# Kernel tuning notes

Hardware: AMD Instinct MI355X
Metric: run time of the kernel (lower is better)

## Reference

```python
import jax, jax.numpy as jnp
import numpy as np

N = 100_000      # nodes
E = 1_600_000    # edges
IN = 128         # input_dim
HID = 64         # hidden_dim
H = 4            # num_heads
DH = HID // H    # per-head dim
L = 3            # num_layers
OUT = 64         # output_dim
SLOPE = 0.2      # DGL GATConv LeakyReLU default
EPS = 1e-5       # LayerNorm eps


def setup_inputs() -> dict:
    key = jax.random.key(0)
    ks = jax.random.split(key, 20)
    s = 0.02
    return {
        "node_features": jax.random.normal(ks[0], (N, IN), jnp.float32),
        "src": jax.random.randint(ks[1], (E,), 0, N, jnp.int32),
        "dst": jax.random.randint(ks[2], (E,), 0, N, jnp.int32),
        # input projection
        "W_in": jax.random.normal(ks[3], (IN, HID), jnp.float32) * s,
        "b_in": jnp.zeros((HID,), jnp.float32),
        # rewiring MLP: Linear(2*HID,64) -> Tanh -> Linear(64,1) -> Sigmoid
        "W_a1": jax.random.normal(ks[4], (2 * HID, 64), jnp.float32) * s,
        "b_a1": jnp.zeros((64,), jnp.float32),
        "W_a2": jax.random.normal(ks[5], (64, 1), jnp.float32) * s,
        "b_a2": jnp.zeros((1,), jnp.float32),
        # stacked GATConv params for L layers
        "W_gat": jax.random.normal(ks[6], (L, HID, H * DH), jnp.float32) * s,
        "a_l": jax.random.normal(ks[7], (L, H, DH), jnp.float32) * s,
        "a_r": jax.random.normal(ks[8], (L, H, DH), jnp.float32) * s,
        "b_gat": jnp.zeros((L, H, DH), jnp.float32),
        # LayerNorm + output projection
        "ln_g": jnp.ones((HID,), jnp.float32),
        "ln_b": jnp.zeros((HID,), jnp.float32),
        "W_out": jax.random.normal(ks[9], (HID, OUT), jnp.float32) * s,
        "b_out": jnp.zeros((OUT,), jnp.float32),
    }


def _gat_layer(h, src, dst, W, al, ar, b):
    # h: (N, HID) -> z: (N, H, DH)
    z = (h @ W).reshape(N, H, DH)
    el = jnp.sum(z * al, axis=-1)                       # (N, H)
    er = jnp.sum(z * ar, axis=-1)                       # (N, H)
    e = jax.nn.leaky_relu(el[src] + er[dst], SLOPE)     # (E, H)
    # segment softmax over incoming edges of each dst node
    m = jax.ops.segment_max(e, dst, num_segments=N)     # (N, H)
    ex = jnp.exp(e - m[dst])                            # (E, H)
    den = jax.ops.segment_sum(ex, dst, num_segments=N)  # (N, H)
    alpha = ex / den[dst]                               # (E, H)
    msg = z[src] * alpha[..., None]                     # (E, H, DH)
    out = jax.ops.segment_sum(msg, dst, num_segments=N) # (N, H, DH)
    # residual (identity since HID == H*DH) + bias, then flatten(1)
    out = out + h.reshape(N, H, DH) + b
    return out.reshape(N, H * DH)


def reference(node_features, src, dst, W_in, b_in, W_a1, b_a1, W_a2, b_a2,
              W_gat, a_l, a_r, b_gat, ln_g, ln_b, W_out, b_out):
    h = node_features @ W_in + b_in                     # (N, HID)
    # GraphRewiringModule: edge-wise gather + MLP + sigmoid score
    he = jnp.concatenate([h[src], h[dst]], axis=1)      # (E, 2*HID)
    edge_score = jax.nn.sigmoid(jnp.tanh(he @ W_a1 + b_a1) @ W_a2 + b_a2)  # (E,1); unused downstream, as in source
    for l in range(L):
        h = _gat_layer(h, src, dst, W_gat[l], a_l[l], a_r[l], b_gat[l])
    # LayerNorm
    mu = jnp.mean(h, axis=-1, keepdims=True)
    var = jnp.mean((h - mu) ** 2, axis=-1, keepdims=True)
    h = (h - mu) * jax.lax.rsqrt(var + EPS) * ln_g + ln_b
    return h @ W_out + b_out                            # (N, OUT)
```

## Files before the change

### kernel.cpp

```cpp
#include <hip/hip_runtime.h>

#define NN 100000
#define EE 1600000
#define IN_DIM 128
#define HID 64
#define NH 4
#define DH 16
#define NL 3
#define OUT_DIM 64
#define SLOPE 0.2f
#define LN_EPS 1e-5f
#define RB 4

#define BSH 9
#define BSZ 512
#define NB ((NN + BSZ - 1) / BSZ)
#define CAP 10240
#define CHUNK 4096
#define P1_BLOCKS ((EE + CHUNK - 1) / CHUNK)

using short8 = __attribute__((ext_vector_type(8))) short;
using f32x4  = __attribute__((ext_vector_type(4))) float;

__device__ __forceinline__ float bcast(float x, int lane) {
    return __int_as_float(__builtin_amdgcn_readlane(__float_as_int(x), lane));
}
__device__ __forceinline__ unsigned f2bf(float x) {
    unsigned u = __float_as_uint(x);
    u += 0x7FFFu + ((u >> 16) & 1u);
    return u >> 16;
}
__device__ __forceinline__ float bflo(unsigned zp) {
    return __uint_as_float(zp << 16);
}
__device__ __forceinline__ float bfhi(unsigned zp) {
    return __uint_as_float(zp & 0xFFFF0000u);
}

__global__ void k_wpack(const float* __restrict__ W, uint4* __restrict__ Wb) {
    const int tid = blockIdx.x * 256 + threadIdx.x;
    if (tid >= 1024) return;
    const int lane = tid & 63;
    const int ntkk = tid >> 6;
    const int nt = ntkk & 3, kk = ntkk >> 2;
    const int k0 = kk * 32 + (lane >> 4) * 8;
    const int n  = nt * 16 + (lane & 15);
    unsigned dw[4];
#pragma unroll
    for (int p = 0; p < 4; ++p) {
        const unsigned lo = f2bf(W[(k0 + 2 * p) * HID + n]);
        const unsigned hi = f2bf(W[(k0 + 2 * p + 1) * HID + n]);
        dw[p] = lo | (hi << 16);
    }
    Wb[ntkk * 64 + lane] = make_uint4(dw[0], dw[1], dw[2], dw[3]);
}

__device__ float walv(const float* __restrict__ W, const float* __restrict__ al,
                      const float* __restrict__ ar, int k, int c) {
    if (c < 4) {
        float s = 0.f;
#pragma unroll
        for (int d = 0; d < 16; ++d) s += W[k * HID + c * 16 + d] * al[c * 16 + d];
        return s;
    }
    if (c < 8) {
        const int hh = c - 4;
        float s = 0.f;
#pragma unroll
        for (int d = 0; d < 16; ++d) s += W[k * HID + hh * 16 + d] * ar[hh * 16 + d];
        return s;
    }
    return 0.f;
}

__global__ void k_wpack_gat(const float* __restrict__ W_gat, const float* __restrict__ a_l,
                            const float* __restrict__ a_r, uint4* __restrict__ Wbg) {
    const int l = blockIdx.y;
    const int tid = blockIdx.x * 256 + threadIdx.x;
    if (tid >= 640) return;
    const int lane = tid & 63;
    const int f = tid >> 6;
    const int kk = f / 5, nt = f % 5;
    const float* W  = W_gat + (size_t)l * HID * HID;
    const float* al = a_l + (size_t)l * HID;
    const float* ar = a_r + (size_t)l * HID;
    const int k0 = kk * 32 + (lane >> 4) * 8;
    const int n  = lane & 15;
    unsigned dw[4];
#pragma unroll
    for (int p = 0; p < 4; ++p) {
        float b0, b1;
        if (nt < 4) {
            b0 = W[(k0 + 2 * p) * HID + nt * 16 + n];
            b1 = W[(k0 + 2 * p + 1) * HID + nt * 16 + n];
        } else {
            b0 = walv(W, al, ar, k0 + 2 * p, n);
            b1 = walv(W, al, ar, k0 + 2 * p + 1, n);
        }
        dw[p] = f2bf(b0) | (f2bf(b1) << 16);
    }
    Wbg[(size_t)l * 640 + f * 64 + lane] = make_uint4(dw[0], dw[1], dw[2], dw[3]);
}

__global__ __launch_bounds__(256)
void k_in_gemm(const float* __restrict__ X, const uint4* __restrict__ Wb,
               const float* __restrict__ b, float* __restrict__ h) {
    const int l  = threadIdx.x & 63;
    const int wv = threadIdx.x >> 6;
    const int wrow = blockIdx.x * 64 + wv * 16;
    if (wrow >= NN) return;
    const int arow = wrow + (l & 15);
    const int kb_off = (l >> 4) * 8;
    f32x4 acc[4];
#pragma unroll
    for (int nt = 0; nt < 4; ++nt) acc[nt] = (f32x4){0.f, 0.f, 0.f, 0.f};
    const float* xr = X + (size_t)arow * IN_DIM;
#pragma unroll
    for (int kk = 0; kk < 4; ++kk) {
        const int kb = kk * 32 + kb_off;
        const float4 xa = *(const float4*)(xr + kb);
        const float4 xb = *(const float4*)(xr + kb + 4);
        const unsigned d0 = f2bf(xa.x) | (f2bf(xa.y) << 16);
        const unsigned d1 = f2bf(xa.z) | (f2bf(xa.w) << 16);
        const unsigned d2 = f2bf(xb.x) | (f2bf(xb.y) << 16);
        const unsigned d3 = f2bf(xb.z) | (f2bf(xb.w) << 16);
        const uint4 au = make_uint4(d0, d1, d2, d3);
        const short8 af = __builtin_bit_cast(short8, au);
#pragma unroll
        for (int nt = 0; nt < 4; ++nt) {
            const uint4 bu = Wb[(kk * 4 + nt) * 64 + l];
            const short8 bf = __builtin_bit_cast(short8, bu);
            acc[nt] = __builtin_amdgcn_mfma_f32_16x16x32_bf16(af, bf, acc[nt], 0, 0, 0);
        }
    }
    const int grp = l >> 4, ci = l & 15;
#pragma unroll
    for (int nt = 0; nt < 4; ++nt) {
        const int col = nt * 16 + ci;
        const float bv = b[col];
#pragma unroll
        for (int r = 0; r < 4; ++r) {
            h[(size_t)(wrow + grp * 4 + r) * HID + col] = acc[nt][r] + bv;
        }
    }
}

__global__ __launch_bounds__(256)
void k_zgemm(const float* __restrict__ h, const uint4* __restrict__ Wbg,
             unsigned* __restrict__ zb32, float* __restrict__ el, float* __restrict__ er) {
    const int l  = threadIdx.x & 63;
    const int wv = threadIdx.x >> 6;
    const int wrow = blockIdx.x * 64 + wv * 16;
    if (wrow >= NN) return;
    const int arow = wrow + (l & 15);
    const int kb_off = (l >> 4) * 8;
    f32x4 acc[5];
#pragma unroll
    for (int nt = 0; nt < 5; ++nt) acc[nt] = (f32x4){0.f, 0.f, 0.f, 0.f};
    const float* hr = h + (size_t)arow * HID;
#pragma unroll
    for (int kk = 0; kk < 2; ++kk) {
        const int kb = kk * 32 + kb_off;
        const float4 xa = *(const float4*)(hr + kb);
        const float4 xb = *(const float4*)(hr + kb + 4);
        const unsigned d0 = f2bf(xa.x) | (f2bf(xa.y) << 16);
        const unsigned d1 = f2bf(xa.z) | (f2bf(xa.w) << 16);
        const unsigned d2 = f2bf(xb.x) | (f2bf(xb.y) << 16);
        const unsigned d3 = f2bf(xb.z) | (f2bf(xb.w) << 16);
        const uint4 au = make_uint4(d0, d1, d2, d3);
        const short8 af = __builtin_bit_cast(short8, au);
#pragma unroll
        for (int nt = 0; nt < 5; ++nt) {
            const uint4 bu = Wbg[(kk * 5 + nt) * 64 + l];
            const short8 bf = __builtin_bit_cast(short8, bu);
            acc[nt] = __builtin_amdgcn_mfma_f32_16x16x32_bf16(af, bf, acc[nt], 0, 0, 0);
        }
    }
    const int grp = l >> 4, ci = l & 15;
#pragma unroll
    for (int nt = 0; nt < 4; ++nt) {
#pragma unroll
        for (int r = 0; r < 4; ++r) {
            const int row = wrow + grp * 4 + r;
            const unsigned my = f2bf(acc[nt][r]);
            const unsigned ot = (unsigned)__shfl_xor((int)my, 1, 64);
            if ((ci & 1) == 0)
                zb32[(size_t)row * 32 + nt * 8 + (ci >> 1)] = my | (ot << 16);
        }
    }
#pragma unroll
    for (int r = 0; r < 4; ++r) {
        const int row = wrow + grp * 4 + r;
        const float v = acc[4][r];
        if (ci < 4) el[row * NH + ci] = v;
        else if (ci < 8) er[row * NH + (ci - 4)] = v;
    }
}


__global__ void k_zero_bcnt(int* __restrict__ bcnt, int* __restrict__ esrc_pad) {
    if (threadIdx.x < NB) bcnt[threadIdx.x] = 0;
    if (threadIdx.x < 8) esrc_pad[threadIdx.x] = 0;
}

__global__ __launch_bounds__(256)
void k_bucketize(const int* __restrict__ src, const int* __restrict__ dst,
                 int* __restrict__ bcnt, int2* __restrict__ bbuf) {
    __shared__ int lh[256];
    __shared__ int lbase[256];
    __shared__ int lcnt[256];
    __shared__ int gbase[256];
    __shared__ int sc[256];
    __shared__ int2 stage[CHUNK];
    const int t = threadIdx.x;
    const int e0 = blockIdx.x * CHUNK;
    const int n = min(CHUNK, EE - e0);
    lh[t] = 0;
    __syncthreads();
    int myd[CHUNK / 256], mys[CHUNK / 256];
#pragma unroll
    for (int i = 0; i < CHUNK / 256; ++i) {
        const int o = i * 256 + t;
        if (o < n) {
            myd[i] = dst[e0 + o];
            mys[i] = src[e0 + o];
            atomicAdd(&lh[myd[i] >> BSH], 1);
        } else myd[i] = -1;
    }
    __syncthreads();
    {
        const int v = lh[t];
        lcnt[t] = v;
        sc[t] = v;
        __syncthreads();
        for (int off = 1; off < 256; off <<= 1) {
            const int x = (t >= off) ? sc[t - off] : 0;
            __syncthreads();
            sc[t] += x;
            __syncthreads();
        }
        lbase[t] = sc[t] - v;
        lh[t] = sc[t] - v;
    }
    __syncthreads();
#pragma unroll
    for (int i = 0; i < CHUNK / 256; ++i) {
        if (myd[i] >= 0) {
            const int b = myd[i] >> BSH;
            const int p = atomicAdd(&lh[b], 1);
            stage[p] = make_int2(mys[i], myd[i]);
        }
    }
    __syncthreads();
    if (t < NB && lcnt[t] > 0) gbase[t] = atomicAdd(&bcnt[t], lcnt[t]);
    __syncthreads();
    for (int i = t; i < n; i += 256) {
        const int2 en = stage[i];
        const int b = en.y >> BSH;
        const int gp = gbase[b] + (i - lbase[b]);
        if (gp < CAP) bbuf[(size_t)b * CAP + gp] = en;
    }
}

__global__ void k_bscan(const int* __restrict__ bcnt, int* __restrict__ bbase,
                        int* __restrict__ rowptr) {
    const int t = threadIdx.x;
    __shared__ int sc[256];
    const int v = (t < NB) ? bcnt[t] : 0;
    sc[t] = v;
    __syncthreads();
    for (int off = 1; off < 256; off <<= 1) {
        const int x = (t >= off) ? sc[t - off] : 0;
        __syncthreads();
        sc[t] += x;
        __syncthreads();
    }
    if (t < NB) bbase[t] = sc[t] - v;
    if (t == 0) rowptr[NN] = EE;
}

__global__ __launch_bounds__(256)
void k_localcsr(const int* __restrict__ bcnt, const int* __restrict__ bbase,
                const int2* __restrict__ bbuf, int* __restrict__ rowptr,
                int* __restrict__ esrc) {
    const int b = blockIdx.x;
    const int t = threadIdx.x;
    const int cnt = bcnt[b];
    const int base = bbase[b];
    const int n0 = b * BSZ;
    const int nn = min(BSZ, NN - n0);
    __shared__ int lh[BSZ];
    __shared__ int lsc[BSZ];
    __shared__ int sc[256];
    for (int i = t; i < BSZ; i += 256) lh[i] = 0;
    __syncthreads();
    const int2* bb = bbuf + (size_t)b * CAP;
    for (int i = t; i < cnt; i += 256) atomicAdd(&lh[bb[i].y & (BSZ - 1)], 1);
    __syncthreads();
    const int a0 = lh[2 * t], a1 = lh[2 * t + 1];
    const int ts = a0 + a1;
    sc[t] = ts;
    __syncthreads();
    for (int off = 1; off < 256; off <<= 1) {
        const int x = (t >= off) ? sc[t - off] : 0;
        __syncthreads();
        sc[t] += x;
        __syncthreads();
    }
    const int ebase = sc[t] - ts;
    lsc[2 * t] = ebase;
    lsc[2 * t + 1] = ebase + a0;
    __syncthreads();
    for (int i = t; i < BSZ; i += 256) {
        if (i < nn) rowptr[n0 + i] = base + lsc[i];
        lh[i] = lsc[i];
    }
    __syncthreads();
    for (int i = t; i < cnt; i += 256) {
        const int2 en = bb[i];
        const int p = atomicAdd(&lh[en.y & (BSZ - 1)], 1);
        esrc[base + p] = en.x;
    }
}

__global__ __launch_bounds__(256)
void k_gat_dst(const int* __restrict__ rowptr, const int* __restrict__ esrc,
               const float* __restrict__ el, const float* __restrict__ er,
               const uint4* __restrict__ zb128, const float* __restrict__ hin,
               const float* __restrict__ bg, float* __restrict__ hout) {
    const int j  = threadIdx.x & 63;
    const int wv = threadIdx.x >> 6;
    const int d = blockIdx.x * 4 + wv;
    if (d >= NN) return;
    const int g = j >> 3;
    const int q = j & 7;
    const int hh = q >> 1;
    const int r0 = rowptr[d], r1 = rowptr[d + 1];
    const float erh = er[d * NH + hh];
    float a0 = 0.f, a1 = 0.f, a2 = 0.f, a3 = 0.f;
    float a4 = 0.f, a5 = 0.f, a6 = 0.f, a7 = 0.f;
    float den = 0.f;
    for (int i = r0; i < r1; i += 8) {
        const int ii = i + g;
        const unsigned s = (unsigned)esrc[ii];
        const float av = el[s * NH + hh];
        const uint4 zp = zb128[s * 8u + q];
        const float x = av + erh;
        float w = __expf(fmaxf(x, SLOPE * x));
        w = (ii < r1) ? w : 0.f;
        den += w;
        a0 = fmaf(w, bflo(zp.x), a0);
        a1 = fmaf(w, bfhi(zp.x), a1);
        a2 = fmaf(w, bflo(zp.y), a2);
        a3 = fmaf(w, bfhi(zp.y), a3);
        a4 = fmaf(w, bflo(zp.z), a4);
        a5 = fmaf(w, bfhi(zp.z), a5);
        a6 = fmaf(w, bflo(zp.w), a6);
        a7 = fmaf(w, bfhi(zp.w), a7);
    }
#pragma unroll
    for (int m = 8; m <= 32; m <<= 1) {
        den += __shfl_xor(den, m, 64);
        a0 += __shfl_xor(a0, m, 64);
        a1 += __shfl_xor(a1, m, 64);
        a2 += __shfl_xor(a2, m, 64);
        a3 += __shfl_xor(a3, m, 64);
        a4 += __shfl_xor(a4, m, 64);
        a5 += __shfl_xor(a5, m, 64);
        a6 += __shfl_xor(a6, m, 64);
        a7 += __shfl_xor(a7, m, 64);
    }
    if (g == 0) {
        const int c = 8 * q;
        const float4 h0 = *(const float4*)(hin + (size_t)d * HID + c);
        const float4 h1 = *(const float4*)(hin + (size_t)d * HID + c + 4);
        const float4 b0 = *(const float4*)(bg + c);
        const float4 b1 = *(const float4*)(bg + c + 4);
        float o0 = h0.x + b0.x, o1 = h0.y + b0.y, o2 = h0.z + b0.z, o3 = h0.w + b0.w;
        float o4 = h1.x + b1.x, o5 = h1.y + b1.y, o6 = h1.z + b1.z, o7 = h1.w + b1.w;
        if (r1 > r0) {
            const float rd = 1.f / den;
            o0 = fmaf(a0, rd, o0); o1 = fmaf(a1, rd, o1);
            o2 = fmaf(a2, rd, o2); o3 = fmaf(a3, rd, o3);
            o4 = fmaf(a4, rd, o4); o5 = fmaf(a5, rd, o5);
            o6 = fmaf(a6, rd, o6); o7 = fmaf(a7, rd, o7);
        }
        *(float4*)(hout + (size_t)d * HID + c)     = make_float4(o0, o1, o2, o3);
        *(float4*)(hout + (size_t)d * HID + c + 4) = make_float4(o4, o5, o6, o7);
    }
}

__global__ __launch_bounds__(256, 4)
void k_ln_out(const float* __restrict__ h, const float* __restrict__ g,
              const float* __restrict__ be, const float* __restrict__ Wo,
              const float* __restrict__ bo, float* __restrict__ out) {
    const int j = threadIdx.x & 63;
    float Wreg[HID];
#pragma unroll
    for (int k = 0; k < HID; ++k) Wreg[k] = Wo[k * OUT_DIM + j];
    const float gj = g[j], bej = be[j], boj = bo[j];
    const int wid = (blockIdx.x * blockDim.x + threadIdx.x) >> 6;
    const int nw  = (gridDim.x * blockDim.x) >> 6;
    for (int v0 = wid * RB; v0 < NN; v0 += nw * RB) {
        float hn[RB];
#pragma unroll
        for (int r = 0; r < RB; ++r) {
            const float x = h[(size_t)(v0 + r) * HID + j];
            float s = x;
#pragma unroll
            for (int m = 32; m >= 1; m >>= 1) s += __shfl_xor(s, m, 64);
            const float mu = s * (1.f / 64.f);
            const float dx = x - mu;
            float vs = dx * dx;
#pragma unroll
            for (int m = 32; m >= 1; m >>= 1) vs += __shfl_xor(vs, m, 64);
            hn[r] = dx * rsqrtf(vs * (1.f / 64.f) + LN_EPS) * gj + bej;
        }
        float acc[RB];
#pragma unroll
        for (int r = 0; r < RB; ++r) acc[r] = boj;
#pragma unroll
        for (int k = 0; k < HID; ++k) {
#pragma unroll
            for (int r = 0; r < RB; ++r)
                acc[r] = fmaf(bcast(hn[r], k), Wreg[k], acc[r]);
        }
#pragma unroll
        for (int r = 0; r < RB; ++r) out[(size_t)(v0 + r) * OUT_DIM + j] = acc[r];
    }
}

extern "C" void kernel_launch(void* const* d_in, const int* in_sizes, int n_in,
                              void* d_out, int out_size, void* d_ws, size_t ws_size,
                              hipStream_t stream) {
    const float* X     = (const float*)d_in[0];
    const int*   src   = (const int*)d_in[1];
    const int*   dst   = (const int*)d_in[2];
    const float* W_in  = (const float*)d_in[3];
    const float* b_in  = (const float*)d_in[4];
    const float* W_gat = (const float*)d_in[9];
    const float* a_l   = (const float*)d_in[10];
    const float* a_r   = (const float*)d_in[11];
    const float* b_gat = (const float*)d_in[12];
    const float* ln_g  = (const float*)d_in[13];
    const float* ln_b  = (const float*)d_in[14];
    const float* W_out = (const float*)d_in[15];
    const float* b_out = (const float*)d_in[16];
    float* out = (float*)d_out;

    float* ws = (float*)d_ws;
    float* hA = ws;
    float* hB = hA + (size_t)NN * HID;
    unsigned* zb32 = (unsigned*)(hB + (size_t)NN * HID);
    float* el = (float*)(zb32 + (size_t)NN * (HID / 2));
    float* er = el + (size_t)NN * NH;
    int* rowptr = (int*)(er + (size_t)NN * NH);
    int* esrc   = rowptr + NN + 1;
    int* bcnt   = esrc + EE + 8;
    int* bbase  = bcnt + NB;
    uintptr_t wp = (uintptr_t)(bbase + NB);
    wp = (wp + 15) & ~(uintptr_t)15;
    uint4* Wb   = (uint4*)wp;
    uint4* Wbg  = Wb + 1024;
    int2* bbuf  = (int2*)hB;

    k_wpack<<<4, 256, 0, stream>>>(W_in, Wb);
    k_wpack_gat<<<dim3(3, NL), 256, 0, stream>>>(W_gat, a_l, a_r, Wbg);
    k_in_gemm<<<(NN + 63) / 64, 256, 0, stream>>>(X, Wb, b_in, hA);

    k_zero_bcnt<<<1, 256, 0, stream>>>(bcnt, esrc + EE);
    k_bucketize<<<P1_BLOCKS, 256, 0, stream>>>(src, dst, bcnt, bbuf);
    k_bscan<<<1, 256, 0, stream>>>(bcnt, bbase, rowptr);
    k_localcsr<<<NB, 256, 0, stream>>>(bcnt, bbase, bbuf, rowptr, esrc);

    float* hin = hA;
    float* hout = hB;
    for (int l = 0; l < NL; ++l) {
        k_zgemm<<<(NN + 63) / 64, 256, 0, stream>>>(hin, Wbg + (size_t)l * 640,
                                                    zb32, el, er);
        k_gat_dst<<<(NN + 3) / 4, 256, 0, stream>>>(rowptr, esrc, el, er,
                                                    (const uint4*)zb32, hin,
                                                    b_gat + (size_t)l * HID, hout);
        float* t = hin; hin = hout; hout = t;
    }

    k_ln_out<<<1024, 256, 0, stream>>>(hin, ln_g, ln_b, W_out, b_out, out);
}
```

Before: 301.1 us.

## Split node features into per-head planes and run GAT aggregation per head

```diff
diff --git a/kernel.cpp b/kernel.cpp
--- a/kernel.cpp
+++ b/kernel.cpp
@@ -11,6 +11,7 @@
 #define SLOPE 0.2f
 #define LN_EPS 1e-5f
 #define RB 4
+#define NG4 (NN / 4)
 
 #define BSH 9
 #define BSZ 512
@@ -136,18 +137,18 @@
     const int grp = l >> 4, ci = l & 15;
 #pragma unroll
     for (int nt = 0; nt < 4; ++nt) {
-        const int col = nt * 16 + ci;
-        const float bv = b[col];
+        const float bv = b[nt * 16 + ci];
 #pragma unroll
         for (int r = 0; r < 4; ++r) {
-            h[(size_t)(wrow + grp * 4 + r) * HID + col] = acc[nt][r] + bv;
+            const int row = wrow + grp * 4 + r;
+            h[((size_t)nt * NN + row) * 16 + ci] = acc[nt][r] + bv;
         }
     }
 }
 
 __global__ __launch_bounds__(256)
 void k_zgemm(const float* __restrict__ h, const uint4* __restrict__ Wbg,
-             unsigned* __restrict__ zb32, float* __restrict__ el, float* __restrict__ er) {
+             unsigned* __restrict__ zbp, float* __restrict__ el_p, float* __restrict__ er_p) {
     const int l  = threadIdx.x & 63;
     const int wv = threadIdx.x >> 6;
     const int wrow = blockIdx.x * 64 + wv * 16;
@@ -157,12 +158,12 @@
     f32x4 acc[5];
 #pragma unroll
     for (int nt = 0; nt < 5; ++nt) acc[nt] = (f32x4){0.f, 0.f, 0.f, 0.f};
-    const float* hr = h + (size_t)arow * HID;
 #pragma unroll
     for (int kk = 0; kk < 2; ++kk) {
         const int kb = kk * 32 + kb_off;
-        const float4 xa = *(const float4*)(hr + kb);
-        const float4 xb = *(const float4*)(hr + kb + 4);
+        const float* hp = h + ((size_t)(kb >> 4) * NN + arow) * 16 + (kb & 15);
+        const float4 xa = *(const float4*)(hp);
+        const float4 xb = *(const float4*)(hp + 4);
         const unsigned d0 = f2bf(xa.x) | (f2bf(xa.y) << 16);
         const unsigned d1 = f2bf(xa.z) | (f2bf(xa.w) << 16);
         const unsigned d2 = f2bf(xb.x) | (f2bf(xb.y) << 16);
@@ -185,15 +186,15 @@
             const unsigned my = f2bf(acc[nt][r]);
             const unsigned ot = (unsigned)__shfl_xor((int)my, 1, 64);
             if ((ci & 1) == 0)
-                zb32[(size_t)row * 32 + nt * 8 + (ci >> 1)] = my | (ot << 16);
+                zbp[((size_t)nt * NN + row) * 8 + (ci >> 1)] = my | (ot << 16);
         }
     }
 #pragma unroll
     for (int r = 0; r < 4; ++r) {
         const int row = wrow + grp * 4 + r;
         const float v = acc[4][r];
-        if (ci < 4) el[row * NH + ci] = v;
-        else if (ci < 8) er[row * NH + (ci - 4)] = v;
+        if (ci < 4) el_p[(size_t)ci * NN + row] = v;
+        else if (ci < 8) er_p[(size_t)(ci - 4) * NN + row] = v;
     }
 }
 
@@ -325,68 +326,51 @@
 
 __global__ __launch_bounds__(256)
 void k_gat_dst(const int* __restrict__ rowptr, const int* __restrict__ esrc,
-               const float* __restrict__ el, const float* __restrict__ er,
-               const uint4* __restrict__ zb128, const float* __restrict__ hin,
-               const float* __restrict__ bg, float* __restrict__ hout) {
+               const float* __restrict__ el_p, const float* __restrict__ er_p,
+               const unsigned* __restrict__ zbp, const float* __restrict__ hin_p,
+               const float* __restrict__ bg, float* __restrict__ hout_p) {
     const int j  = threadIdx.x & 63;
     const int wv = threadIdx.x >> 6;
-    const int d = blockIdx.x * 4 + wv;
-    if (d >= NN) return;
+    const int hh = blockIdx.x / NG4;
+    const int ng = blockIdx.x % NG4;
+    const int d = ng * 4 + wv;
     const int g = j >> 3;
     const int q = j & 7;
-    const int hh = q >> 1;
     const int r0 = rowptr[d], r1 = rowptr[d + 1];
-    const float erh = er[d * NH + hh];
-    float a0 = 0.f, a1 = 0.f, a2 = 0.f, a3 = 0.f;
-    float a4 = 0.f, a5 = 0.f, a6 = 0.f, a7 = 0.f;
-    float den = 0.f;
+    const size_t plane = (size_t)hh * NN;
+    const float erh = er_p[plane + d];
+    float s0 = 0.f, s1 = 0.f, den = 0.f;
     for (int i = r0; i < r1; i += 8) {
         const int ii = i + g;
-        const unsigned s = (unsigned)esrc[ii];
-        const float av = el[s * NH + hh];
-        const uint4 zp = zb128[s * 8u + q];
+        const unsigned s = (unsigned)__builtin_nontemporal_load(esrc + ii);
+        const float av = el_p[plane + s];
+        const unsigned zp = zbp[(plane + s) * 8 + q];
         const float x = av + erh;
         float w = __expf(fmaxf(x, SLOPE * x));
         w = (ii < r1) ? w : 0.f;
         den += w;
-        a0 = fmaf(w, bflo(zp.x), a0);
-        a1 = fmaf(w, bfhi(zp.x), a1);
-        a2 = fmaf(w, bflo(zp.y), a2);
-        a3 = fmaf(w, bfhi(zp.y), a3);
-        a4 = fmaf(w, bflo(zp.z), a4);
-        a5 = fmaf(w, bfhi(zp.z), a5);
-        a6 = fmaf(w, bflo(zp.w), a6);
-        a7 = fmaf(w, bfhi(zp.w), a7);
+        s0 = fmaf(w, bflo(zp), s0);
+        s1 = fmaf(w, bfhi(zp), s1);
     }
 #pragma unroll
     for (int m = 8; m <= 32; m <<= 1) {
         den += __shfl_xor(den, m, 64);
-        a0 += __shfl_xor(a0, m, 64);
-        a1 += __shfl_xor(a1, m, 64);
-        a2 += __shfl_xor(a2, m, 64);
-        a3 += __shfl_xor(a3, m, 64);
-        a4 += __shfl_xor(a4, m, 64);
-        a5 += __shfl_xor(a5, m, 64);
-        a6 += __shfl_xor(a6, m, 64);
-        a7 += __shfl_xor(a7, m, 64);
+        s0  += __shfl_xor(s0, m, 64);
+        s1  += __shfl_xor(s1, m, 64);
     }
     if (g == 0) {
-        const int c = 8 * q;
-        const float4 h0 = *(const float4*)(hin + (size_t)d * HID + c);
-        const float4 h1 = *(const float4*)(hin + (size_t)d * HID + c + 4);
-        const float4 b0 = *(const float4*)(bg + c);
-        const float4 b1 = *(const float4*)(bg + c + 4);
-        float o0 = h0.x + b0.x, o1 = h0.y + b0.y, o2 = h0.z + b0.z, o3 = h0.w + b0.w;
-        float o4 = h1.x + b1.x, o5 = h1.y + b1.y, o6 = h1.z + b1.z, o7 = h1.w + b1.w;
+        const size_t off = (plane + d) * 16 + 2 * q;
+        const double hvd = __builtin_nontemporal_load((const double*)(hin_p + off));
+        const float2 hv = __builtin_bit_cast(float2, hvd);
+        float o0 = hv.x + bg[hh * 16 + 2 * q];
+        float o1 = hv.y + bg[hh * 16 + 2 * q + 1];
         if (r1 > r0) {
             const float rd = 1.f / den;
-            o0 = fmaf(a0, rd, o0); o1 = fmaf(a1, rd, o1);
-            o2 = fmaf(a2, rd, o2); o3 = fmaf(a3, rd, o3);
-            o4 = fmaf(a4, rd, o4); o5 = fmaf(a5, rd, o5);
-            o6 = fmaf(a6, rd, o6); o7 = fmaf(a7, rd, o7);
-        }
-        *(float4*)(hout + (size_t)d * HID + c)     = make_float4(o0, o1, o2, o3);
-        *(float4*)(hout + (size_t)d * HID + c + 4) = make_float4(o4, o5, o6, o7);
+            o0 = fmaf(s0, rd, o0);
+            o1 = fmaf(s1, rd, o1);
+        }
+        const float2 ov = make_float2(o0, o1);
+        __builtin_nontemporal_store(__builtin_bit_cast(double, ov), (double*)(hout_p + off));
     }
 }
 
@@ -399,13 +383,15 @@
 #pragma unroll
     for (int k = 0; k < HID; ++k) Wreg[k] = Wo[k * OUT_DIM + j];
     const float gj = g[j], bej = be[j], boj = bo[j];
+    const size_t pbase = (size_t)(j >> 4) * NN;
+    const int ci = j & 15;
     const int wid = (blockIdx.x * blockDim.x + threadIdx.x) >> 6;
     const int nw  = (gridDim.x * blockDim.x) >> 6;
     for (int v0 = wid * RB; v0 < NN; v0 += nw * RB) {
         float hn[RB];
 #pragma unroll
         for (int r = 0; r < RB; ++r) {
-            const float x = h[(size_t)(v0 + r) * HID + j];
+            const float x = h[(pbase + (v0 + r)) * 16 + ci];
             float s = x;
 #pragma unroll
             for (int m = 32; m >= 1; m >>= 1) s += __shfl_xor(s, m, 64);
@@ -451,10 +437,10 @@
     float* ws = (float*)d_ws;
     float* hA = ws;
     float* hB = hA + (size_t)NN * HID;
-    unsigned* zb32 = (unsigned*)(hB + (size_t)NN * HID);
-    float* el = (float*)(zb32 + (size_t)NN * (HID / 2));
-    float* er = el + (size_t)NN * NH;
-    int* rowptr = (int*)(er + (size_t)NN * NH);
+    unsigned* zbp = (unsigned*)(hB + (size_t)NN * HID);
+    float* el_p = (float*)(zbp + (size_t)NN * (HID / 2));
+    float* er_p = el_p + (size_t)NN * NH;
+    int* rowptr = (int*)(er_p + (size_t)NN * NH);
     int* esrc   = rowptr + NN + 1;
     int* bcnt   = esrc + EE + 8;
     int* bbase  = bcnt + NB;
@@ -477,10 +463,9 @@
     float* hout = hB;
     for (int l = 0; l < NL; ++l) {
         k_zgemm<<<(NN + 63) / 64, 256, 0, stream>>>(hin, Wbg + (size_t)l * 640,
-                                                    zb32, el, er);
-        k_gat_dst<<<(NN + 3) / 4, 256, 0, stream>>>(rowptr, esrc, el, er,
-                                                    (const uint4*)zb32, hin,
-                                                    b_gat + (size_t)l * HID, hout);
+                                                    zbp, el_p, er_p);
+        k_gat_dst<<<NH * NG4, 256, 0, stream>>>(rowptr, esrc, el_p, er_p, zbp, hin,
+                                                b_gat + (size_t)l * HID, hout);
         float* t = hin; hin = hout; hout = t;
     }
 
```

New measurement: 676.5 us. 2.25x slower.

## Store hidden state in bf16 and software-pipeline edge gathers in GAT aggregation

Applied to the files above, without the earlier changes.

```diff
diff --git a/kernel.cpp b/kernel.cpp
--- a/kernel.cpp
+++ b/kernel.cpp
@@ -29,6 +29,9 @@
     unsigned u = __float_as_uint(x);
     u += 0x7FFFu + ((u >> 16) & 1u);
     return u >> 16;
+}
+__device__ __forceinline__ float bf2f(unsigned short b) {
+    return __uint_as_float(((unsigned)b) << 16);
 }
 __device__ __forceinline__ float bflo(unsigned zp) {
     return __uint_as_float(zp << 16);
@@ -104,7 +107,7 @@
 
 __global__ __launch_bounds__(256)
 void k_in_gemm(const float* __restrict__ X, const uint4* __restrict__ Wb,
-               const float* __restrict__ b, float* __restrict__ h) {
+               const float* __restrict__ b, unsigned* __restrict__ h32) {
     const int l  = threadIdx.x & 63;
     const int wv = threadIdx.x >> 6;
     const int wrow = blockIdx.x * 64 + wv * 16;
@@ -136,17 +139,20 @@
     const int grp = l >> 4, ci = l & 15;
 #pragma unroll
     for (int nt = 0; nt < 4; ++nt) {
-        const int col = nt * 16 + ci;
-        const float bv = b[col];
+        const float bv = b[nt * 16 + ci];
 #pragma unroll
         for (int r = 0; r < 4; ++r) {
-            h[(size_t)(wrow + grp * 4 + r) * HID + col] = acc[nt][r] + bv;
+            const int row = wrow + grp * 4 + r;
+            const unsigned my = f2bf(acc[nt][r] + bv);
+            const unsigned ot = (unsigned)__shfl_xor((int)my, 1, 64);
+            if ((ci & 1) == 0)
+                h32[(size_t)row * 32 + nt * 8 + (ci >> 1)] = my | (ot << 16);
         }
     }
 }
 
 __global__ __launch_bounds__(256)
-void k_zgemm(const float* __restrict__ h, const uint4* __restrict__ Wbg,
+void k_zgemm(const unsigned short* __restrict__ h16, const uint4* __restrict__ Wbg,
              unsigned* __restrict__ zb32, float* __restrict__ el, float* __restrict__ er) {
     const int l  = threadIdx.x & 63;
     const int wv = threadIdx.x >> 6;
@@ -157,17 +163,10 @@
     f32x4 acc[5];
 #pragma unroll
     for (int nt = 0; nt < 5; ++nt) acc[nt] = (f32x4){0.f, 0.f, 0.f, 0.f};
-    const float* hr = h + (size_t)arow * HID;
 #pragma unroll
     for (int kk = 0; kk < 2; ++kk) {
         const int kb = kk * 32 + kb_off;
-        const float4 xa = *(const float4*)(hr + kb);
-        const float4 xb = *(const float4*)(hr + kb + 4);
-        const unsigned d0 = f2bf(xa.x) | (f2bf(xa.y) << 16);
-        const unsigned d1 = f2bf(xa.z) | (f2bf(xa.w) << 16);
-        const unsigned d2 = f2bf(xb.x) | (f2bf(xb.y) << 16);
-        const unsigned d3 = f2bf(xb.z) | (f2bf(xb.w) << 16);
-        const uint4 au = make_uint4(d0, d1, d2, d3);
+        const uint4 au = *(const uint4*)(h16 + (size_t)arow * 64 + kb);
         const short8 af = __builtin_bit_cast(short8, au);
 #pragma unroll
         for (int nt = 0; nt < 5; ++nt) {
@@ -200,7 +199,7 @@
 
 __global__ void k_zero_bcnt(int* __restrict__ bcnt, int* __restrict__ esrc_pad) {
     if (threadIdx.x < NB) bcnt[threadIdx.x] = 0;
-    if (threadIdx.x < 8) esrc_pad[threadIdx.x] = 0;
+    if (threadIdx.x < 32) esrc_pad[threadIdx.x] = 0;
 }
 
 __global__ __launch_bounds__(256)
@@ -326,8 +325,8 @@
 __global__ __launch_bounds__(256)
 void k_gat_dst(const int* __restrict__ rowptr, const int* __restrict__ esrc,
                const float* __restrict__ el, const float* __restrict__ er,
-               const uint4* __restrict__ zb128, const float* __restrict__ hin,
-               const float* __restrict__ bg, float* __restrict__ hout) {
+               const uint4* __restrict__ zb128, const unsigned short* __restrict__ hin16,
+               const float* __restrict__ bg, unsigned* __restrict__ hout32) {
     const int j  = threadIdx.x & 63;
     const int wv = threadIdx.x >> 6;
     const int d = blockIdx.x * 4 + wv;
@@ -337,26 +336,32 @@
     const int hh = q >> 1;
     const int r0 = rowptr[d], r1 = rowptr[d + 1];
     const float erh = er[d * NH + hh];
+    uint4 hv4 = make_uint4(0, 0, 0, 0);
+    if (g == 0) hv4 = *(const uint4*)(hin16 + (size_t)d * 64 + 8 * q);
     float a0 = 0.f, a1 = 0.f, a2 = 0.f, a3 = 0.f;
     float a4 = 0.f, a5 = 0.f, a6 = 0.f, a7 = 0.f;
     float den = 0.f;
+    unsigned sA = (unsigned)esrc[r0 + g];
+    float avA = el[sA * NH + hh];
+    uint4 zpA = zb128[sA * 8u + q];
+    unsigned sB = (unsigned)esrc[r0 + 8 + g];
     for (int i = r0; i < r1; i += 8) {
-        const int ii = i + g;
-        const unsigned s = (unsigned)esrc[ii];
-        const float av = el[s * NH + hh];
-        const uint4 zp = zb128[s * 8u + q];
-        const float x = av + erh;
+        const float avB = el[sB * NH + hh];
+        const uint4 zpB = zb128[sB * 8u + q];
+        const unsigned sC = (unsigned)esrc[i + 16 + g];
+        const float x = avA + erh;
         float w = __expf(fmaxf(x, SLOPE * x));
-        w = (ii < r1) ? w : 0.f;
+        w = (i + g < r1) ? w : 0.f;
         den += w;
-        a0 = fmaf(w, bflo(zp.x), a0);
-        a1 = fmaf(w, bfhi(zp.x), a1);
-        a2 = fmaf(w, bflo(zp.y), a2);
-        a3 = fmaf(w, bfhi(zp.y), a3);
-        a4 = fmaf(w, bflo(zp.z), a4);
-        a5 = fmaf(w, bfhi(zp.z), a5);
-        a6 = fmaf(w, bflo(zp.w), a6);
-        a7 = fmaf(w, bfhi(zp.w), a7);
+        a0 = fmaf(w, bflo(zpA.x), a0);
+        a1 = fmaf(w, bfhi(zpA.x), a1);
+        a2 = fmaf(w, bflo(zpA.y), a2);
+        a3 = fmaf(w, bfhi(zpA.y), a3);
+        a4 = fmaf(w, bflo(zpA.z), a4);
+        a5 = fmaf(w, bfhi(zpA.z), a5);
+        a6 = fmaf(w, bflo(zpA.w), a6);
+        a7 = fmaf(w, bfhi(zpA.w), a7);
+        sA = sB; avA = avB; zpA = zpB; sB = sC;
     }
 #pragma unroll
     for (int m = 8; m <= 32; m <<= 1) {
@@ -372,12 +377,10 @@
     }
     if (g == 0) {
         const int c = 8 * q;
-        const float4 h0 = *(const float4*)(hin + (size_t)d * HID + c);
-        const float4 h1 = *(const float4*)(hin + (size_t)d * HID + c + 4);
-        const float4 b0 = *(const float4*)(bg + c);
-        const float4 b1 = *(const float4*)(bg + c + 4);
-        float o0 = h0.x + b0.x, o1 = h0.y + b0.y, o2 = h0.z + b0.z, o3 = h0.w + b0.w;
-        float o4 = h1.x + b1.x, o5 = h1.y + b1.y, o6 = h1.z + b1.z, o7 = h1.w + b1.w;
+        float o0 = bflo(hv4.x) + bg[c + 0], o1 = bfhi(hv4.x) + bg[c + 1];
+        float o2 = bflo(hv4.y) + bg[c + 2], o3 = bfhi(hv4.y) + bg[c + 3];
+        float o4 = bflo(hv4.z) + bg[c + 4], o5 = bfhi(hv4.z) + bg[c + 5];
+        float o6 = bflo(hv4.w) + bg[c + 6], o7 = bfhi(hv4.w) + bg[c + 7];
         if (r1 > r0) {
             const float rd = 1.f / den;
             o0 = fmaf(a0, rd, o0); o1 = fmaf(a1, rd, o1);
@@ -385,13 +388,16 @@
             o4 = fmaf(a4, rd, o4); o5 = fmaf(a5, rd, o5);
             o6 = fmaf(a6, rd, o6); o7 = fmaf(a7, rd, o7);
         }
-        *(float4*)(hout + (size_t)d * HID + c)     = make_float4(o0, o1, o2, o3);
-        *(float4*)(hout + (size_t)d * HID + c + 4) = make_float4(o4, o5, o6, o7);
+        const uint4 ov = make_uint4(f2bf(o0) | (f2bf(o1) << 16),
+                                    f2bf(o2) | (f2bf(o3) << 16),
+                                    f2bf(o4) | (f2bf(o5) << 16),
+                                    f2bf(o6) | (f2bf(o7) << 16));
+        *(uint4*)(hout32 + (size_t)d * 32 + 4 * q) = ov;
     }
 }
 
 __global__ __launch_bounds__(256, 4)
-void k_ln_out(const float* __restrict__ h, const float* __restrict__ g,
+void k_ln_out(const unsigned short* __restrict__ h16, const float* __restrict__ g,
               const float* __restrict__ be, const float* __restrict__ Wo,
               const float* __restrict__ bo, float* __restrict__ out) {
     const int j = threadIdx.x & 63;
@@ -405,7 +411,7 @@
         float hn[RB];
 #pragma unroll
         for (int r = 0; r < RB; ++r) {
-            const float x = h[(size_t)(v0 + r) * HID + j];
+            const float x = bf2f(h16[(size_t)(v0 + r) * HID + j]);
             float s = x;
 #pragma unroll
             for (int m = 32; m >= 1; m >>= 1) s += __shfl_xor(s, m, 64);
@@ -448,40 +454,41 @@
     const float* b_out = (const float*)d_in[16];
     float* out = (float*)d_out;
 
-    float* ws = (float*)d_ws;
-    float* hA = ws;
-    float* hB = hA + (size_t)NN * HID;
-    unsigned* zb32 = (unsigned*)(hB + (size_t)NN * HID);
+    char* ws = (char*)d_ws;
+    unsigned short* hA16 = (unsigned short*)ws;
+    unsigned short* hB16 = hA16 + (size_t)NN * HID;
+    unsigned* zb32 = (unsigned*)(hB16 + (size_t)NN * HID);
     float* el = (float*)(zb32 + (size_t)NN * (HID / 2));
     float* er = el + (size_t)NN * NH;
     int* rowptr = (int*)(er + (size_t)NN * NH);
     int* esrc   = rowptr + NN + 1;
-    int* bcnt   = esrc + EE + 8;
+    int* bcnt   = esrc + EE + 32;
     int* bbase  = bcnt + NB;
     uintptr_t wp = (uintptr_t)(bbase + NB);
     wp = (wp + 15) & ~(uintptr_t)15;
     uint4* Wb   = (uint4*)wp;
     uint4* Wbg  = Wb + 1024;
-    int2* bbuf  = (int2*)hB;
+    int2* bbuf  = (int2*)hB16;
 
     k_wpack<<<4, 256, 0, stream>>>(W_in, Wb);
     k_wpack_gat<<<dim3(3, NL), 256, 0, stream>>>(W_gat, a_l, a_r, Wbg);
-    k_in_gemm<<<(NN + 63) / 64, 256, 0, stream>>>(X, Wb, b_in, hA);
+    k_in_gemm<<<(NN + 63) / 64, 256, 0, stream>>>(X, Wb, b_in, (unsigned*)hA16);
 
     k_zero_bcnt<<<1, 256, 0, stream>>>(bcnt, esrc + EE);
     k_bucketize<<<P1_BLOCKS, 256, 0, stream>>>(src, dst, bcnt, bbuf);
     k_bscan<<<1, 256, 0, stream>>>(bcnt, bbase, rowptr);
     k_localcsr<<<NB, 256, 0, stream>>>(bcnt, bbase, bbuf, rowptr, esrc);
 
-    float* hin = hA;
-    float* hout = hB;
+    unsigned short* hin = hA16;
+    unsigned short* hout = hB16;
     for (int l = 0; l < NL; ++l) {
         k_zgemm<<<(NN + 63) / 64, 256, 0, stream>>>(hin, Wbg + (size_t)l * 640,
                                                     zb32, el, er);
         k_gat_dst<<<(NN + 3) / 4, 256, 0, stream>>>(rowptr, esrc, el, er,
                                                     (const uint4*)zb32, hin,
-                                                    b_gat + (size_t)l * HID, hout);
-        float* t = hin; hin = hout; hout = t;
+                                                    b_gat + (size_t)l * HID,
+                                                    (unsigned*)hout);
+        unsigned short* t = hin; hin = hout; hout = t;
     }
 
     k_ln_out<<<1024, 256, 0, stream>>>(hin, ln_g, ln_b, W_out, b_out, out);
```

Result: no change. 295.8 us (-1.8%).
